# Kernel tuning notes

Hardware: AMD Instinct MI355X
Metric: run time of the kernel (lower is better)

The kernel has to match this reference:

```python
import jax, jax.numpy as jnp
import numpy as np

N = 100000   # nodes
E = 1600000  # edges
IN, H, C = 128, 128, 64
LN_EPS = 1e-5


def _xavier(key, fan_in, fan_out):
    lim = jnp.sqrt(6.0 / (fan_in + fan_out)).astype(jnp.float32)
    return jax.random.uniform(key, (fan_in, fan_out), jnp.float32, -lim, lim)


def setup_inputs() -> dict:
    key = jax.random.key(0)
    ks = jax.random.split(key, 6)
    feats = jax.random.normal(ks[0], (N, IN), jnp.float32)
    src = jax.random.randint(ks[1], (E,), 0, N, jnp.int32)
    dst = jax.random.randint(ks[2], (E,), 0, N, jnp.int32)
    return {
        "feats": feats, "src": src, "dst": dst,
        "W0": _xavier(ks[3], IN, H), "b0": jnp.zeros((H,), jnp.float32),
        "g0": jnp.ones((H,), jnp.float32), "be0": jnp.zeros((H,), jnp.float32),
        "W1": _xavier(ks[4], H, H), "b1": jnp.zeros((H,), jnp.float32),
        "g1": jnp.ones((H,), jnp.float32), "be1": jnp.zeros((H,), jnp.float32),
        "W2": _xavier(ks[5], H, C), "b2": jnp.zeros((C,), jnp.float32),
    }


def _gcn_agg(h, src, dst):
    # symmetric GCN normalization: out[v] = sum_{(u,v) in E} h[u] / sqrt(deg_out(u) * deg_in(v))
    ones = jnp.ones(src.shape, jnp.float32)
    deg_out = jax.ops.segment_sum(ones, src, num_segments=N)
    deg_in = jax.ops.segment_sum(ones, dst, num_segments=N)
    norm_o = jax.lax.rsqrt(jnp.maximum(deg_out, 1.0))
    norm_i = jax.lax.rsqrt(jnp.maximum(deg_in, 1.0))
    msg = (h * norm_o[:, None])[src]                       # [E, d] gather
    agg = jax.ops.segment_sum(msg, dst, num_segments=N)    # [N, d] scatter-add
    return agg * norm_i[:, None]


def _layernorm(x, gamma, beta):
    mu = jnp.mean(x, axis=-1, keepdims=True)
    var = jnp.mean(jnp.square(x - mu), axis=-1, keepdims=True)
    return (x - mu) * jax.lax.rsqrt(var + LN_EPS) * gamma + beta


def reference(feats, src, dst, W0, b0, g0, be0, W1, b1, g1, be1, W2, b2):
    # layer 0: agg -> matmul -> bias -> dropout(eval: identity) -> layernorm -> relu
    h = _gcn_agg(feats, src, dst) @ W0 + b0
    h = jax.nn.relu(_layernorm(h, g0, be0))
    # layer 1
    h = _gcn_agg(h, src, dst) @ W1 + b1
    h = jax.nn.relu(_layernorm(h, g1, be1))
    # final layer: agg -> matmul -> bias
    out = _gcn_agg(h, src, dst) @ W2 + b2
    return out
```

## Files before the change

### kernel.cpp

```cpp
#include <hip/hip_runtime.h>
#include <hip/hip_fp16.h>

constexpr float LN_EPS = 1e-5f;

typedef _Float16 f16x8 __attribute__((ext_vector_type(8)));
typedef float f32x4 __attribute__((ext_vector_type(4)));

__device__ __forceinline__ unsigned short f2h(float f) {
  return __half_as_ushort(__float2half_rn(f));
}
__device__ __forceinline__ unsigned int pk2h(float x, float y) {
  return (unsigned int)f2h(x) | ((unsigned int)f2h(y) << 16);
}
__device__ __forceinline__ __half2 u2h2(unsigned int u) {
  return *reinterpret_cast<__half2*>(&u);
}

#define NPB 256
#define CHUNK 4096

__global__ __launch_bounds__(256) void passA_kernel(
    const int* __restrict__ src, const int* __restrict__ dst,
    int* __restrict__ cntD, int* __restrict__ cntS, int NB, int NBLK, int E) {
  extern __shared__ int sh[];
  for (int j = threadIdx.x; j < 2 * NB; j += 256) sh[j] = 0;
  __syncthreads();
  const int blk = blockIdx.x;
  const int base = blk * CHUNK;
  const int end = min(base + CHUNK, E);
  const int cnt = end - base;
  const int nv = cnt >> 2;
  const int4* d4p = reinterpret_cast<const int4*>(dst + base);
  const int4* s4p = reinterpret_cast<const int4*>(src + base);
  for (int q = threadIdx.x; q < nv; q += 256) {
    int4 d4 = d4p[q];
    int4 s4 = s4p[q];
    atomicAdd(&sh[d4.x >> 8], 1); atomicAdd(&sh[d4.y >> 8], 1);
    atomicAdd(&sh[d4.z >> 8], 1); atomicAdd(&sh[d4.w >> 8], 1);
    atomicAdd(&sh[NB + (s4.x >> 8)], 1); atomicAdd(&sh[NB + (s4.y >> 8)], 1);
    atomicAdd(&sh[NB + (s4.z >> 8)], 1); atomicAdd(&sh[NB + (s4.w >> 8)], 1);
  }
  for (int i = (nv << 2) + threadIdx.x; i < cnt; i += 256) {
    atomicAdd(&sh[dst[base + i] >> 8], 1);
    atomicAdd(&sh[NB + (src[base + i] >> 8)], 1);
  }
  __syncthreads();
  for (int j = threadIdx.x; j < NB; j += 256) {
    cntD[j * NBLK + blk] = sh[j];
    cntS[j * NBLK + blk] = sh[NB + j];
  }
}

__global__ __launch_bounds__(512) void scan1_kernel(
    const int* __restrict__ cntD, const int* __restrict__ cntS,
    int* __restrict__ offLD, int* __restrict__ offLS,
    int* __restrict__ totD, int* __restrict__ totS, int NB, int NBLK) {
  __shared__ int p[512];
  const int t = threadIdx.x;
  const bool isS = blockIdx.x >= NB;
  const int b = isS ? blockIdx.x - NB : blockIdx.x;
  const int* cnt = isS ? cntS : cntD;
  int* offL = isS ? offLS : offLD;
  int own = (t < NBLK) ? cnt[b * NBLK + t] : 0;
  p[t] = own;
  __syncthreads();
  for (int off = 1; off < 512; off <<= 1) {
    int x = (t >= off) ? p[t - off] : 0;
    __syncthreads();
    p[t] += x;
    __syncthreads();
  }
  if (t < NBLK) offL[b * NBLK + t] = p[t] - own;
  if (t == 511) (isS ? totS : totD)[b] = p[511];
}

__global__ __launch_bounds__(512) void scan2_kernel(
    const int* __restrict__ totD, const int* __restrict__ totS,
    int* __restrict__ bktD, int* __restrict__ bktS,
    int* __restrict__ row_st, int NB, int N, int E) {
  __shared__ int p[512];
  const int t = threadIdx.x;
  int own = (t < NB) ? totD[t] : 0;
  p[t] = own;
  __syncthreads();
  for (int off = 1; off < 512; off <<= 1) {
    int x = (t >= off) ? p[t - off] : 0;
    __syncthreads();
    p[t] += x;
    __syncthreads();
  }
  if (t < NB) bktD[t] = p[t] - own;
  __syncthreads();
  int own2 = (t < NB) ? totS[t] : 0;
  p[t] = own2;
  __syncthreads();
  for (int off = 1; off < 512; off <<= 1) {
    int x = (t >= off) ? p[t - off] : 0;
    __syncthreads();
    p[t] += x;
    __syncthreads();
  }
  if (t < NB) bktS[t] = p[t] - own2;
  if (t == 0) {
    bktD[NB] = E;
    bktS[NB] = E;
    row_st[N] = E;
  }
}

__global__ __launch_bounds__(256) void passB_kernel(
    const int* __restrict__ src, const int* __restrict__ dst,
    const int* __restrict__ cntD, const int* __restrict__ cntS,
    const int* __restrict__ offLD, const int* __restrict__ offLS,
    const int* __restrict__ bkt_stD, const int* __restrict__ bkt_stS,
    unsigned int* __restrict__ packedD, unsigned char* __restrict__ srcS,
    int NB, int NBLK, int E) {
  __shared__ unsigned int sD[CHUNK];
  __shared__ unsigned short bD_[CHUNK];
  __shared__ unsigned char sS_[CHUNK];
  __shared__ unsigned short bS_[CHUNK];
  __shared__ int hD[512], lD[512], hS[512], lS[512];
  const int t = threadIdx.x;
  const int blk = blockIdx.x;
  const int base = blk * CHUNK;
  const int end = min(base + CHUNK, E);
  const int cnt = end - base;
  hD[t] = (t < NB) ? cntD[t * NBLK + blk] : 0;
  hD[t + 256] = (t + 256 < NB) ? cntD[(t + 256) * NBLK + blk] : 0;
  hS[t] = (t < NB) ? cntS[t * NBLK + blk] : 0;
  hS[t + 256] = (t + 256 < NB) ? cntS[(t + 256) * NBLK + blk] : 0;
  __syncthreads();
  int oD0 = hD[t], oD1 = hD[t + 256], oS0 = hS[t], oS1 = hS[t + 256];
  for (int off = 1; off < 512; off <<= 1) {
    int xd0 = (t >= off) ? hD[t - off] : 0;
    int xd1 = (t + 256 >= off) ? hD[t + 256 - off] : 0;
    int xs0 = (t >= off) ? hS[t - off] : 0;
    int xs1 = (t + 256 >= off) ? hS[t + 256 - off] : 0;
    __syncthreads();
    hD[t] += xd0; hD[t + 256] += xd1;
    hS[t] += xs0; hS[t + 256] += xs1;
    __syncthreads();
  }
  lD[t] = hD[t] - oD0; lD[t + 256] = hD[t + 256] - oD1;
  lS[t] = hS[t] - oS0; lS[t + 256] = hS[t + 256] - oS1;
  __syncthreads();
  hD[t] = lD[t]; hD[t + 256] = lD[t + 256];
  hS[t] = lS[t]; hS[t + 256] = lS[t + 256];
  __syncthreads();
  const int nv = cnt >> 2;
  const int4* d4p = reinterpret_cast<const int4*>(dst + base);
  const int4* s4p = reinterpret_cast<const int4*>(src + base);
  for (int q = t; q < nv; q += 256) {
    int4 d4 = d4p[q];
    int4 s4 = s4p[q];
#pragma unroll
    for (int k = 0; k < 4; ++k) {
      const int d = (&d4.x)[k];
      const int s = (&s4.x)[k];
      const int bD = d >> 8;
      const int pD = atomicAdd(&hD[bD], 1);
      sD[pD] = ((unsigned int)(d & 255) << 24) | (unsigned int)s;
      bD_[pD] = (unsigned short)bD;
      const int bS = s >> 8;
      const int pS = atomicAdd(&hS[bS], 1);
      sS_[pS] = (unsigned char)(s & 255);
      bS_[pS] = (unsigned short)bS;
    }
  }
  for (int i = (nv << 2) + t; i < cnt; i += 256) {
    const int d = dst[base + i];
    const int s = src[base + i];
    const int bD = d >> 8;
    const int pD = atomicAdd(&hD[bD], 1);
    sD[pD] = ((unsigned int)(d & 255) << 24) | (unsigned int)s;
    bD_[pD] = (unsigned short)bD;
    const int bS = s >> 8;
    const int pS = atomicAdd(&hS[bS], 1);
    sS_[pS] = (unsigned char)(s & 255);
    bS_[pS] = (unsigned short)bS;
  }
  __syncthreads();
  for (int i = t; i < cnt; i += 256) {
    const int bD = bD_[i];
    packedD[bkt_stD[bD] + offLD[bD * NBLK + blk] + (i - lD[bD])] = sD[i];
    const int bS = bS_[i];
    srcS[bkt_stS[bS] + offLS[bS * NBLK + blk] + (i - lS[bS])] = sS_[i];
  }
}

__global__ __launch_bounds__(256) void passC_kernel(
    const unsigned int* __restrict__ packed, const int* __restrict__ bucket_start,
    int* __restrict__ row_st, float* __restrict__ ni,
    int* __restrict__ edge_src, int N) {
  __shared__ int cnt[NPB];
  __shared__ int cur[NPB];
  __shared__ int tmp[NPB];
  const int b = blockIdx.x;
  const int t = threadIdx.x;
  const int v0 = b * NPB;
  const int bs = bucket_start[b];
  const int be = bucket_start[b + 1];
  cnt[t] = 0;
  __syncthreads();
  const int a0 = bs + ((4 - (bs & 3)) & 3);
  const int a1 = a0 + (((be - a0) >> 2) << 2);
  for (int i = bs + t; i < min(a0, be); i += 256)
    atomicAdd(&cnt[packed[i] >> 24], 1);
  const uint4* p4 = reinterpret_cast<const uint4*>(packed + a0);
  const int nv = (a1 - a0) >> 2;
  for (int q = t; q < nv; q += 256) {
    uint4 p = p4[q];
    atomicAdd(&cnt[p.x >> 24], 1); atomicAdd(&cnt[p.y >> 24], 1);
    atomicAdd(&cnt[p.z >> 24], 1); atomicAdd(&cnt[p.w >> 24], 1);
  }
  for (int i = max(a1, bs) + t; i < be; i += 256)
    atomicAdd(&cnt[packed[i] >> 24], 1);
  __syncthreads();
  int own = cnt[t];
  tmp[t] = own;
  __syncthreads();
  for (int off = 1; off < NPB; off <<= 1) {
    int x = (t >= off) ? tmp[t - off] : 0;
    __syncthreads();
    tmp[t] += x;
    __syncthreads();
  }
  const int pref = tmp[t] - own;
  if (v0 + t < N) {
    row_st[v0 + t] = bs + pref;
    ni[v0 + t] = rsqrtf(fmaxf((float)own, 1.0f));
  }
  cur[t] = bs + pref;
  __syncthreads();
  for (int i = bs + t; i < min(a0, be); i += 256) {
    unsigned int p = packed[i];
    int pos = atomicAdd(&cur[p >> 24], 1);
    edge_src[pos] = (int)(p & 0xFFFFFFu);
  }
  for (int q = t; q < nv; q += 256) {
    uint4 p = p4[q];
#pragma unroll
    for (int k = 0; k < 4; ++k) {
      unsigned int pv = (&p.x)[k];
      int pos = atomicAdd(&cur[pv >> 24], 1);
      edge_src[pos] = (int)(pv & 0xFFFFFFu);
    }
  }
  for (int i = max(a1, bs) + t; i < be; i += 256) {
    unsigned int p = packed[i];
    int pos = atomicAdd(&cur[p >> 24], 1);
    edge_src[pos] = (int)(p & 0xFFFFFFu);
  }
}

__global__ __launch_bounds__(256) void passD_kernel(
    const unsigned char* __restrict__ srcS, const int* __restrict__ bkt_stS,
    float* __restrict__ no, int N) {
  __shared__ int cnt[NPB];
  const int b = blockIdx.x;
  const int t = threadIdx.x;
  cnt[t] = 0;
  __syncthreads();
  const int bs = bkt_stS[b];
  const int be = bkt_stS[b + 1];
  for (int i = bs + t; i < be; i += 256)
    atomicAdd(&cnt[srcS[i]], 1);
  __syncthreads();
  const int v = b * NPB + t;
  if (v < N) no[v] = rsqrtf(fmaxf((float)cnt[t], 1.0f));
}

__global__ void wconv_kernel(const float* __restrict__ W, unsigned short* __restrict__ Wt,
                             int K, int C) {
  int i = blockIdx.x * blockDim.x + threadIdx.x;
  if (i < K * C) {
    int k = i / C, c = i - k * C;
    Wt[c * K + k] = f2h(W[i]);
  }
}

__global__ __launch_bounds__(256) void featconv_kernel(const float* __restrict__ F,
                                                       const float* __restrict__ no,
                                                       unsigned short* __restrict__ out, int N) {
  int row = blockIdx.x * 8 + (threadIdx.x >> 5);
  if (row >= N) return;
  int c = (threadIdx.x & 31) * 4;
  float4 v = *reinterpret_cast<const float4*>(F + (size_t)row * 128 + c);
  float nof = no[row];
  uint2 p = {pk2h(v.x * nof, v.y * nof), pk2h(v.z * nof, v.w * nof)};
  *reinterpret_cast<uint2*>(out + (size_t)row * 128 + c) = p;
}

__global__ __launch_bounds__(256) void gather_agg_h(
    const unsigned short* __restrict__ hH, const int* __restrict__ row_start,
    const int* __restrict__ edge_src, const float* __restrict__ ni,
    unsigned short* __restrict__ aggH, int N) {
  const int v = blockIdx.x * 4 + (threadIdx.x >> 6);
  if (v >= N) return;
  const int l = threadIdx.x & 63;
  const int half = l >> 5;
  const int lane = l & 31;
  const int s = row_start[v];
  const int e = row_start[v + 1];
  const int co = 4 * lane;
  const __half2 z = __float2half2_rn(0.f);
  __half2 A0 = z, A1 = z, B0 = z, B1 = z, C0 = z, C1 = z, D0 = z, D1 = z;
  int j = s;
  for (; j + 8 <= e; j += 8) {
    int u0 = edge_src[j + half];
    int u1 = edge_src[j + 2 + half];
    int u2 = edge_src[j + 4 + half];
    int u3 = edge_src[j + 6 + half];
    uint2 p0 = *reinterpret_cast<const uint2*>(hH + (size_t)u0 * 128 + co);
    uint2 p1 = *reinterpret_cast<const uint2*>(hH + (size_t)u1 * 128 + co);
    uint2 p2 = *reinterpret_cast<const uint2*>(hH + (size_t)u2 * 128 + co);
    uint2 p3 = *reinterpret_cast<const uint2*>(hH + (size_t)u3 * 128 + co);
    A0 = __hadd2(A0, u2h2(p0.x)); A1 = __hadd2(A1, u2h2(p0.y));
    B0 = __hadd2(B0, u2h2(p1.x)); B1 = __hadd2(B1, u2h2(p1.y));
    C0 = __hadd2(C0, u2h2(p2.x)); C1 = __hadd2(C1, u2h2(p2.y));
    D0 = __hadd2(D0, u2h2(p3.x)); D1 = __hadd2(D1, u2h2(p3.y));
  }
  for (; j + 2 <= e; j += 2) {
    int u0 = edge_src[j + half];
    uint2 p0 = *reinterpret_cast<const uint2*>(hH + (size_t)u0 * 128 + co);
    A0 = __hadd2(A0, u2h2(p0.x)); A1 = __hadd2(A1, u2h2(p0.y));
  }
  if (j < e && half == 0) {
    int u0 = edge_src[j];
    uint2 p0 = *reinterpret_cast<const uint2*>(hH + (size_t)u0 * 128 + co);
    A0 = __hadd2(A0, u2h2(p0.x)); A1 = __hadd2(A1, u2h2(p0.y));
  }
  float a0 = (__low2float(A0) + __low2float(B0)) + (__low2float(C0) + __low2float(D0));
  float a1 = (__high2float(A0) + __high2float(B0)) + (__high2float(C0) + __high2float(D0));
  float a2 = (__low2float(A1) + __low2float(B1)) + (__low2float(C1) + __low2float(D1));
  float a3 = (__high2float(A1) + __high2float(B1)) + (__high2float(C1) + __high2float(D1));
  a0 += __shfl_xor(a0, 32);
  a1 += __shfl_xor(a1, 32);
  a2 += __shfl_xor(a2, 32);
  a3 += __shfl_xor(a3, 32);
  if (half == 0) {
    const float niv = ni[v];
    uint2 po = {pk2h(a0 * niv, a1 * niv), pk2h(a2 * niv, a3 * niv)};
    *reinterpret_cast<uint2*>(aggH + (size_t)v * 128 + co) = po;
  }
}

__global__ __launch_bounds__(256) void gather_out(
    const unsigned short* __restrict__ zH, const int* __restrict__ row_start,
    const int* __restrict__ edge_src, const float* __restrict__ ni,
    const float* __restrict__ bias, float* __restrict__ out, int N) {
  const int v = blockIdx.x * 4 + (threadIdx.x >> 6);
  if (v >= N) return;
  const int l = threadIdx.x & 63;
  const int half = l >> 5;
  const int lane = l & 31;
  const int s = row_start[v];
  const int e = row_start[v + 1];
  const int co = 2 * lane;
  const __half2 z = __float2half2_rn(0.f);
  __half2 A = z, B = z, C = z, D = z;
  int j = s;
  for (; j + 8 <= e; j += 8) {
    int u0 = edge_src[j + half];
    int u1 = edge_src[j + 2 + half];
    int u2 = edge_src[j + 4 + half];
    int u3 = edge_src[j + 6 + half];
    A = __hadd2(A, u2h2(*reinterpret_cast<const unsigned int*>(zH + (size_t)u0 * 64 + co)));
    B = __hadd2(B, u2h2(*reinterpret_cast<const unsigned int*>(zH + (size_t)u1 * 64 + co)));
    C = __hadd2(C, u2h2(*reinterpret_cast<const unsigned int*>(zH + (size_t)u2 * 64 + co)));
    D = __hadd2(D, u2h2(*reinterpret_cast<const unsigned int*>(zH + (size_t)u3 * 64 + co)));
  }
  for (; j + 2 <= e; j += 2) {
    int u0 = edge_src[j + half];
    A = __hadd2(A, u2h2(*reinterpret_cast<const unsigned int*>(zH + (size_t)u0 * 64 + co)));
  }
  if (j < e && half == 0) {
    int u0 = edge_src[j];
    A = __hadd2(A, u2h2(*reinterpret_cast<const unsigned int*>(zH + (size_t)u0 * 64 + co)));
  }
  float a0 = (__low2float(A) + __low2float(B)) + (__low2float(C) + __low2float(D));
  float a1 = (__high2float(A) + __high2float(B)) + (__high2float(C) + __high2float(D));
  a0 += __shfl_xor(a0, 32);
  a1 += __shfl_xor(a1, 32);
  if (half == 0) {
    const float niv = ni[v];
    float2 bb = *reinterpret_cast<const float2*>(bias + co);
    float2 w = {a0 * niv + bb.x, a1 * niv + bb.y};
    *reinterpret_cast<float2*>(out + (size_t)v * 64 + co) = w;
  }
}

__global__ __launch_bounds__(256) void mm_mfma_ln(
    const unsigned short* __restrict__ A, const unsigned short* __restrict__ Wt,
    const float* __restrict__ b, const float* __restrict__ g,
    const float* __restrict__ be, const float* __restrict__ no,
    unsigned short* __restrict__ out, int N) {
  __shared__ float sS[2][2][16];
  __shared__ float sQ[2][2][16];
  __shared__ float sNo[32];
  const int rbase = blockIdx.x * 32;
  const int w = threadIdx.x >> 6;
  const int l = threadIdx.x & 63;
  const int rt = w & 1, ch = w >> 1;
  if (threadIdx.x < 32) sNo[threadIdx.x] = no[min(rbase + (int)threadIdx.x, N - 1)];
  const int arow = min(rbase + rt * 16 + (l & 15), N - 1);
  const int kof = (l >> 4) * 8;

  f16x8 af[4];
  const unsigned short* ap = A + (size_t)arow * 128 + kof;
#pragma unroll
  for (int kk = 0; kk < 4; ++kk)
    af[kk] = *reinterpret_cast<const f16x8*>(ap + kk * 32);

  f32x4 acc[4] = {};
#pragma unroll
  for (int ct = 0; ct < 4; ++ct) {
    const int ccol = ch * 64 + ct * 16 + (l & 15);
    const unsigned short* bp = Wt + (size_t)ccol * 128 + kof;
#pragma unroll
    for (int kk = 0; kk < 4; ++kk) {
      f16x8 bfr = *reinterpret_cast<const f16x8*>(bp + kk * 32);
      acc[ct] = __builtin_amdgcn_mfma_f32_16x16x32_f16(af[kk], bfr, acc[ct], 0, 0, 0);
    }
  }

  float s[4] = {0.f, 0.f, 0.f, 0.f}, q[4] = {0.f, 0.f, 0.f, 0.f};
#pragma unroll
  for (int ct = 0; ct < 4; ++ct) {
    const float bc = b[ch * 64 + ct * 16 + (l & 15)];
#pragma unroll
    for (int j = 0; j < 4; ++j) {
      float v = acc[ct][j] + bc;
      acc[ct][j] = v;
      s[j] += v;
      q[j] += v * v;
    }
  }
#pragma unroll
  for (int j = 0; j < 4; ++j) {
#pragma unroll
    for (int off = 1; off < 16; off <<= 1) {
      s[j] += __shfl_xor(s[j], off);
      q[j] += __shfl_xor(q[j], off);
    }
  }
  const int grp = l >> 4;
  if ((l & 15) == 0) {
#pragma unroll
    for (int j = 0; j < 4; ++j) {
      sS[rt][ch][grp * 4 + j] = s[j];
      sQ[rt][ch][grp * 4 + j] = q[j];
    }
  }
  __syncthreads();

#pragma unroll
  for (int j = 0; j < 4; ++j) {
    const int r = grp * 4 + j;
    const int row = rbase + rt * 16 + r;
    float S = sS[rt][0][r] + sS[rt][1][r];
    float Q = sQ[rt][0][r] + sQ[rt][1][r];
    float mu = S * (1.f / 128.f);
    float rstd = rsqrtf(fmaxf(Q * (1.f / 128.f) - mu * mu, 0.f) + LN_EPS);
    float nof = sNo[rt * 16 + r];
    if (row < N) {
#pragma unroll
      for (int ct = 0; ct < 4; ++ct) {
        const int ccol = ch * 64 + ct * 16 + (l & 15);
        float y = (acc[ct][j] - mu) * rstd * g[ccol] + be[ccol];
        y = fmaxf(y, 0.f) * nof;
        out[(size_t)row * 128 + ccol] = f2h(y);
      }
    }
  }
}

__global__ __launch_bounds__(256) void mm_z_mfma(
    const unsigned short* __restrict__ A, const unsigned short* __restrict__ Wt,
    unsigned short* __restrict__ zH, int N) {
  const int rbase = blockIdx.x * 32;
  const int w = threadIdx.x >> 6;
  const int l = threadIdx.x & 63;
  const int rt = w & 1, ch = w >> 1;
  const int arow = min(rbase + rt * 16 + (l & 15), N - 1);
  const int kof = (l >> 4) * 8;

  f16x8 af[4];
  const unsigned short* ap = A + (size_t)arow * 128 + kof;
#pragma unroll
  for (int kk = 0; kk < 4; ++kk)
    af[kk] = *reinterpret_cast<const f16x8*>(ap + kk * 32);

  f32x4 acc[2] = {};
#pragma unroll
  for (int ct = 0; ct < 2; ++ct) {
    const int ccol = ch * 32 + ct * 16 + (l & 15);
    const unsigned short* bp = Wt + (size_t)ccol * 128 + kof;
#pragma unroll
    for (int kk = 0; kk < 4; ++kk) {
      f16x8 bfr = *reinterpret_cast<const f16x8*>(bp + kk * 32);
      acc[ct] = __builtin_amdgcn_mfma_f32_16x16x32_f16(af[kk], bfr, acc[ct], 0, 0, 0);
    }
  }
  const int grp = l >> 4;
#pragma unroll
  for (int ct = 0; ct < 2; ++ct) {
    const int ccol = ch * 32 + ct * 16 + (l & 15);
#pragma unroll
    for (int j = 0; j < 4; ++j) {
      const int row = rbase + rt * 16 + grp * 4 + j;
      if (row < N) zH[(size_t)row * 64 + ccol] = f2h(acc[ct][j]);
    }
  }
}

extern "C" void kernel_launch(void* const* d_in, const int* in_sizes, int n_in,
                              void* d_out, int out_size, void* d_ws, size_t ws_size,
                              hipStream_t stream) {
  const float* feats = (const float*)d_in[0];
  const int*   src   = (const int*)d_in[1];
  const int*   dst   = (const int*)d_in[2];
  const float* W0    = (const float*)d_in[3];
  const float* b0    = (const float*)d_in[4];
  const float* g0    = (const float*)d_in[5];
  const float* be0   = (const float*)d_in[6];
  const float* W1    = (const float*)d_in[7];
  const float* b1    = (const float*)d_in[8];
  const float* g1    = (const float*)d_in[9];
  const float* be1   = (const float*)d_in[10];
  const float* W2    = (const float*)d_in[11];
  const float* b2    = (const float*)d_in[12];
  float* out = (float*)d_out;

  const int n = in_sizes[0] / 128;
  const int e = in_sizes[1];
  const int NB = (n + NPB - 1) / NPB;
  const int NBLK = (e + CHUNK - 1) / CHUNK;

  float* ws = (float*)d_ws;
  auto pad4 = [](size_t x) { return (x + 3) & ~(size_t)3; };
  size_t o = 0;
  float* norm_o  = ws + o; o = pad4(o + n);
  float* norm_i  = ws + o; o = pad4(o + n);
  int*   cntD    = (int*)(ws + o); o = pad4(o + (size_t)NB * NBLK);
  int*   cntS    = (int*)(ws + o); o = pad4(o + (size_t)NB * NBLK);
  int*   offLD   = (int*)(ws + o); o = pad4(o + (size_t)NB * NBLK);
  int*   offLS   = (int*)(ws + o); o = pad4(o + (size_t)NB * NBLK);
  int*   totD    = (int*)(ws + o); o = pad4(o + NB);
  int*   totS    = (int*)(ws + o); o = pad4(o + NB);
  int*   bkt_stD = (int*)(ws + o); o = pad4(o + NB + 1);
  int*   bkt_stS = (int*)(ws + o); o = pad4(o + NB + 1);
  int*   row_st  = (int*)(ws + o); o = pad4(o + n + 1);
  unsigned int*  packedD = (unsigned int*)(ws + o);  o = pad4(o + (size_t)e);
  unsigned char* srcS    = (unsigned char*)(ws + o); o = pad4(o + (size_t)(e + 3) / 4);
  int*   edg_src = (int*)(ws + o); o = pad4(o + (size_t)e);
  unsigned short* featH = (unsigned short*)(ws + o); o = pad4(o + (size_t)n * 64);
  unsigned short* aggH  = (unsigned short*)(ws + o); o = pad4(o + (size_t)n * 64);
  unsigned short* Wt0   = (unsigned short*)(ws + o); o = pad4(o + 128 * 128 / 2);
  unsigned short* Wt1   = (unsigned short*)(ws + o); o = pad4(o + 128 * 128 / 2);
  unsigned short* Wt2   = (unsigned short*)(ws + o); o = pad4(o + 128 * 64 / 2);
  unsigned short* hH = featH;
  unsigned short* zH = aggH;

  passA_kernel<<<NBLK, 256, 2 * NB * sizeof(int), stream>>>(src, dst, cntD, cntS, NB, NBLK, e);
  scan1_kernel<<<2 * NB, 512, 0, stream>>>(cntD, cntS, offLD, offLS, totD, totS, NB, NBLK);
  scan2_kernel<<<1, 512, 0, stream>>>(totD, totS, bkt_stD, bkt_stS, row_st, NB, n, e);
  passB_kernel<<<NBLK, 256, 0, stream>>>(src, dst, cntD, cntS, offLD, offLS, bkt_stD, bkt_stS,
                                         packedD, srcS, NB, NBLK, e);
  passC_kernel<<<NB, 256, 0, stream>>>(packedD, bkt_stD, row_st, norm_i, edg_src, n);
  passD_kernel<<<NB, 256, 0, stream>>>(srcS, bkt_stS, norm_o, n);

  wconv_kernel<<<(128 * 128 + 255) / 256, 256, 0, stream>>>(W0, Wt0, 128, 128);
  wconv_kernel<<<(128 * 128 + 255) / 256, 256, 0, stream>>>(W1, Wt1, 128, 128);
  wconv_kernel<<<(128 * 64 + 255) / 256, 256, 0, stream>>>(W2, Wt2, 128, 64);
  featconv_kernel<<<(n + 7) / 8, 256, 0, stream>>>(feats, norm_o, featH, n);

  const int gblocks = (n + 3) / 4;
  const int mblocks = (n + 31) / 32;

  gather_agg_h<<<gblocks, 256, 0, stream>>>(featH, row_st, edg_src, norm_i, aggH, n);
  mm_mfma_ln<<<mblocks, 256, 0, stream>>>(aggH, Wt0, b0, g0, be0, norm_o, hH, n);
  gather_agg_h<<<gblocks, 256, 0, stream>>>(hH, row_st, edg_src, norm_i, aggH, n);
  mm_mfma_ln<<<mblocks, 256, 0, stream>>>(aggH, Wt1, b1, g1, be1, norm_o, hH, n);
  mm_z_mfma<<<mblocks, 256, 0, stream>>>(hH, Wt2, zH, n);
  gather_out<<<gblocks, 256, 0, stream>>>(zH, row_st, edg_src, norm_i, b2, out, n);
}
```

Measured before the change: 388.9 us.

## Slice gathers by feature columns and fuse layer-1 LN with final matmul

Gather kernels now split the feature dimension into 16-column slices, with grid blocks ordered slice-major. Each wave walks 8 nodes with 8 edge groups per node, so concurrently running blocks touch only a narrow slice of the source feature table, which is meant to improve L2 hit rate on random gathers. The layer-1 matmul+LayerNorm is fused with the W2 projection through a shared-memory tile, removing one kernel and a round trip of the hidden activations. In exchange, each edge index is read once per slice and each gather load is only 4 bytes, and the per-node loop is serial with more shuffle reductions.

```diff
diff --git a/kernel.cpp b/kernel.cpp
--- a/kernel.cpp
+++ b/kernel.cpp
@@ -291,102 +291,74 @@
   *reinterpret_cast<uint2*>(out + (size_t)row * 128 + c) = p;
 }
 
-__global__ __launch_bounds__(256) void gather_agg_h(
+__global__ __launch_bounds__(256) void gather_slice(
     const unsigned short* __restrict__ hH, const int* __restrict__ row_start,
     const int* __restrict__ edge_src, const float* __restrict__ ni,
-    unsigned short* __restrict__ aggH, int N) {
-  const int v = blockIdx.x * 4 + (threadIdx.x >> 6);
-  if (v >= N) return;
+    unsigned short* __restrict__ aggH, int N, int gblocks) {
+  const int slice = blockIdx.x / gblocks;
+  const int nb = blockIdx.x - slice * gblocks;
+  const int w = threadIdx.x >> 6;
   const int l = threadIdx.x & 63;
-  const int half = l >> 5;
-  const int lane = l & 31;
-  const int s = row_start[v];
-  const int e = row_start[v + 1];
-  const int co = 4 * lane;
-  const __half2 z = __float2half2_rn(0.f);
-  __half2 A0 = z, A1 = z, B0 = z, B1 = z, C0 = z, C1 = z, D0 = z, D1 = z;
-  int j = s;
-  for (; j + 8 <= e; j += 8) {
-    int u0 = edge_src[j + half];
-    int u1 = edge_src[j + 2 + half];
-    int u2 = edge_src[j + 4 + half];
-    int u3 = edge_src[j + 6 + half];
-    uint2 p0 = *reinterpret_cast<const uint2*>(hH + (size_t)u0 * 128 + co);
-    uint2 p1 = *reinterpret_cast<const uint2*>(hH + (size_t)u1 * 128 + co);
-    uint2 p2 = *reinterpret_cast<const uint2*>(hH + (size_t)u2 * 128 + co);
-    uint2 p3 = *reinterpret_cast<const uint2*>(hH + (size_t)u3 * 128 + co);
-    A0 = __hadd2(A0, u2h2(p0.x)); A1 = __hadd2(A1, u2h2(p0.y));
-    B0 = __hadd2(B0, u2h2(p1.x)); B1 = __hadd2(B1, u2h2(p1.y));
-    C0 = __hadd2(C0, u2h2(p2.x)); C1 = __hadd2(C1, u2h2(p2.y));
-    D0 = __hadd2(D0, u2h2(p3.x)); D1 = __hadd2(D1, u2h2(p3.y));
-  }
-  for (; j + 2 <= e; j += 2) {
-    int u0 = edge_src[j + half];
-    uint2 p0 = *reinterpret_cast<const uint2*>(hH + (size_t)u0 * 128 + co);
-    A0 = __hadd2(A0, u2h2(p0.x)); A1 = __hadd2(A1, u2h2(p0.y));
-  }
-  if (j < e && half == 0) {
-    int u0 = edge_src[j];
-    uint2 p0 = *reinterpret_cast<const uint2*>(hH + (size_t)u0 * 128 + co);
-    A0 = __hadd2(A0, u2h2(p0.x)); A1 = __hadd2(A1, u2h2(p0.y));
-  }
-  float a0 = (__low2float(A0) + __low2float(B0)) + (__low2float(C0) + __low2float(D0));
-  float a1 = (__high2float(A0) + __high2float(B0)) + (__high2float(C0) + __high2float(D0));
-  float a2 = (__low2float(A1) + __low2float(B1)) + (__low2float(C1) + __low2float(D1));
-  float a3 = (__high2float(A1) + __high2float(B1)) + (__high2float(C1) + __high2float(D1));
-  a0 += __shfl_xor(a0, 32);
-  a1 += __shfl_xor(a1, 32);
-  a2 += __shfl_xor(a2, 32);
-  a3 += __shfl_xor(a3, 32);
-  if (half == 0) {
-    const float niv = ni[v];
-    uint2 po = {pk2h(a0 * niv, a1 * niv), pk2h(a2 * niv, a3 * niv)};
-    *reinterpret_cast<uint2*>(aggH + (size_t)v * 128 + co) = po;
-  }
-}
-
-__global__ __launch_bounds__(256) void gather_out(
+  const int grp = l >> 3;
+  const int lane = l & 7;
+  const int co = slice * 16 + lane * 2;
+  const int vbase = nb * 32 + w * 8;
+  const __half2 zz = __float2half2_rn(0.f);
+#pragma unroll 1
+  for (int k = 0; k < 8; ++k) {
+    const int v = vbase + k;
+    if (v >= N) break;
+    const int s = row_start[v];
+    const int e = row_start[v + 1];
+    __half2 acc = zz;
+    for (int j = s + grp; j < e; j += 8)
+      acc = __hadd2(acc, u2h2(*reinterpret_cast<const unsigned int*>(
+                        hH + (size_t)edge_src[j] * 128 + co)));
+    float a0 = __low2float(acc), a1 = __high2float(acc);
+    a0 += __shfl_xor(a0, 8);  a1 += __shfl_xor(a1, 8);
+    a0 += __shfl_xor(a0, 16); a1 += __shfl_xor(a1, 16);
+    a0 += __shfl_xor(a0, 32); a1 += __shfl_xor(a1, 32);
+    if (grp == 0) {
+      const float niv = ni[v];
+      *reinterpret_cast<unsigned int*>(aggH + (size_t)v * 128 + co) =
+          pk2h(a0 * niv, a1 * niv);
+    }
+  }
+}
+
+__global__ __launch_bounds__(256) void gather_out_slice(
     const unsigned short* __restrict__ zH, const int* __restrict__ row_start,
     const int* __restrict__ edge_src, const float* __restrict__ ni,
-    const float* __restrict__ bias, float* __restrict__ out, int N) {
-  const int v = blockIdx.x * 4 + (threadIdx.x >> 6);
-  if (v >= N) return;
+    const float* __restrict__ bias, float* __restrict__ out, int N, int gblocks) {
+  const int slice = blockIdx.x / gblocks;
+  const int nb = blockIdx.x - slice * gblocks;
+  const int w = threadIdx.x >> 6;
   const int l = threadIdx.x & 63;
-  const int half = l >> 5;
-  const int lane = l & 31;
-  const int s = row_start[v];
-  const int e = row_start[v + 1];
-  const int co = 2 * lane;
-  const __half2 z = __float2half2_rn(0.f);
-  __half2 A = z, B = z, C = z, D = z;
-  int j = s;
-  for (; j + 8 <= e; j += 8) {
-    int u0 = edge_src[j + half];
-    int u1 = edge_src[j + 2 + half];
-    int u2 = edge_src[j + 4 + half];
-    int u3 = edge_src[j + 6 + half];
-    A = __hadd2(A, u2h2(*reinterpret_cast<const unsigned int*>(zH + (size_t)u0 * 64 + co)));
-    B = __hadd2(B, u2h2(*reinterpret_cast<const unsigned int*>(zH + (size_t)u1 * 64 + co)));
-    C = __hadd2(C, u2h2(*reinterpret_cast<const unsigned int*>(zH + (size_t)u2 * 64 + co)));
-    D = __hadd2(D, u2h2(*reinterpret_cast<const unsigned int*>(zH + (size_t)u3 * 64 + co)));
-  }
-  for (; j + 2 <= e; j += 2) {
-    int u0 = edge_src[j + half];
-    A = __hadd2(A, u2h2(*reinterpret_cast<const unsigned int*>(zH + (size_t)u0 * 64 + co)));
-  }
-  if (j < e && half == 0) {
-    int u0 = edge_src[j];
-    A = __hadd2(A, u2h2(*reinterpret_cast<const unsigned int*>(zH + (size_t)u0 * 64 + co)));
-  }
-  float a0 = (__low2float(A) + __low2float(B)) + (__low2float(C) + __low2float(D));
-  float a1 = (__high2float(A) + __high2float(B)) + (__high2float(C) + __high2float(D));
-  a0 += __shfl_xor(a0, 32);
-  a1 += __shfl_xor(a1, 32);
-  if (half == 0) {
-    const float niv = ni[v];
-    float2 bb = *reinterpret_cast<const float2*>(bias + co);
-    float2 w = {a0 * niv + bb.x, a1 * niv + bb.y};
-    *reinterpret_cast<float2*>(out + (size_t)v * 64 + co) = w;
+  const int grp = l >> 3;
+  const int lane = l & 7;
+  const int co = slice * 16 + lane * 2;
+  const int vbase = nb * 32 + w * 8;
+  const __half2 zz = __float2half2_rn(0.f);
+#pragma unroll 1
+  for (int k = 0; k < 8; ++k) {
+    const int v = vbase + k;
+    if (v >= N) break;
+    const int s = row_start[v];
+    const int e = row_start[v + 1];
+    __half2 acc = zz;
+    for (int j = s + grp; j < e; j += 8)
+      acc = __hadd2(acc, u2h2(*reinterpret_cast<const unsigned int*>(
+                        zH + (size_t)edge_src[j] * 64 + co)));
+    float a0 = __low2float(acc), a1 = __high2float(acc);
+    a0 += __shfl_xor(a0, 8);  a1 += __shfl_xor(a1, 8);
+    a0 += __shfl_xor(a0, 16); a1 += __shfl_xor(a1, 16);
+    a0 += __shfl_xor(a0, 32); a1 += __shfl_xor(a1, 32);
+    if (grp == 0) {
+      const float niv = ni[v];
+      float2 bb = *reinterpret_cast<const float2*>(bias + co);
+      float2 o = {a0 * niv + bb.x, a1 * niv + bb.y};
+      *reinterpret_cast<float2*>(out + (size_t)v * 64 + co) = o;
+    }
   }
 }
 
@@ -475,13 +447,20 @@
   }
 }
 
-__global__ __launch_bounds__(256) void mm_z_mfma(
+__global__ __launch_bounds__(256) void mm_ln_z(
     const unsigned short* __restrict__ A, const unsigned short* __restrict__ Wt,
-    unsigned short* __restrict__ zH, int N) {
+    const float* __restrict__ b, const float* __restrict__ g,
+    const float* __restrict__ be, const float* __restrict__ no,
+    const unsigned short* __restrict__ Wt2, unsigned short* __restrict__ zH, int N) {
+  __shared__ float sS[2][2][16];
+  __shared__ float sQ[2][2][16];
+  __shared__ float sNo[32];
+  __shared__ unsigned short ht[32][136];
   const int rbase = blockIdx.x * 32;
   const int w = threadIdx.x >> 6;
   const int l = threadIdx.x & 63;
   const int rt = w & 1, ch = w >> 1;
+  if (threadIdx.x < 32) sNo[threadIdx.x] = no[min(rbase + (int)threadIdx.x, N - 1)];
   const int arow = min(rbase + rt * 16 + (l & 15), N - 1);
   const int kof = (l >> 4) * 8;
 
@@ -491,10 +470,10 @@
   for (int kk = 0; kk < 4; ++kk)
     af[kk] = *reinterpret_cast<const f16x8*>(ap + kk * 32);
 
-  f32x4 acc[2] = {};
-#pragma unroll
-  for (int ct = 0; ct < 2; ++ct) {
-    const int ccol = ch * 32 + ct * 16 + (l & 15);
+  f32x4 acc[4] = {};
+#pragma unroll
+  for (int ct = 0; ct < 4; ++ct) {
+    const int ccol = ch * 64 + ct * 16 + (l & 15);
     const unsigned short* bp = Wt + (size_t)ccol * 128 + kof;
 #pragma unroll
     for (int kk = 0; kk < 4; ++kk) {
@@ -502,14 +481,78 @@
       acc[ct] = __builtin_amdgcn_mfma_f32_16x16x32_f16(af[kk], bfr, acc[ct], 0, 0, 0);
     }
   }
+
+  float s[4] = {0.f, 0.f, 0.f, 0.f}, q[4] = {0.f, 0.f, 0.f, 0.f};
+#pragma unroll
+  for (int ct = 0; ct < 4; ++ct) {
+    const float bc = b[ch * 64 + ct * 16 + (l & 15)];
+#pragma unroll
+    for (int j = 0; j < 4; ++j) {
+      float v = acc[ct][j] + bc;
+      acc[ct][j] = v;
+      s[j] += v;
+      q[j] += v * v;
+    }
+  }
+#pragma unroll
+  for (int j = 0; j < 4; ++j) {
+#pragma unroll
+    for (int off = 1; off < 16; off <<= 1) {
+      s[j] += __shfl_xor(s[j], off);
+      q[j] += __shfl_xor(q[j], off);
+    }
+  }
   const int grp = l >> 4;
+  if ((l & 15) == 0) {
+#pragma unroll
+    for (int j = 0; j < 4; ++j) {
+      sS[rt][ch][grp * 4 + j] = s[j];
+      sQ[rt][ch][grp * 4 + j] = q[j];
+    }
+  }
+  __syncthreads();
+
+#pragma unroll
+  for (int j = 0; j < 4; ++j) {
+    const int r = grp * 4 + j;
+    float S = sS[rt][0][r] + sS[rt][1][r];
+    float Q = sQ[rt][0][r] + sQ[rt][1][r];
+    float mu = S * (1.f / 128.f);
+    float rstd = rsqrtf(fmaxf(Q * (1.f / 128.f) - mu * mu, 0.f) + LN_EPS);
+    float nof = sNo[rt * 16 + r];
+#pragma unroll
+    for (int ct = 0; ct < 4; ++ct) {
+      const int ccol = ch * 64 + ct * 16 + (l & 15);
+      float y = (acc[ct][j] - mu) * rstd * g[ccol] + be[ccol];
+      y = fmaxf(y, 0.f) * nof;
+      ht[rt * 16 + r][ccol] = f2h(y);
+    }
+  }
+  __syncthreads();
+
+  f16x8 af2[4];
+#pragma unroll
+  for (int kk = 0; kk < 4; ++kk)
+    af2[kk] = *reinterpret_cast<const f16x8*>(&ht[rt * 16 + (l & 15)][kof + kk * 32]);
+
+  f32x4 acc2[2] = {};
 #pragma unroll
   for (int ct = 0; ct < 2; ++ct) {
     const int ccol = ch * 32 + ct * 16 + (l & 15);
+    const unsigned short* bp = Wt2 + (size_t)ccol * 128 + kof;
+#pragma unroll
+    for (int kk = 0; kk < 4; ++kk) {
+      f16x8 bfr = *reinterpret_cast<const f16x8*>(bp + kk * 32);
+      acc2[ct] = __builtin_amdgcn_mfma_f32_16x16x32_f16(af2[kk], bfr, acc2[ct], 0, 0, 0);
+    }
+  }
+#pragma unroll
+  for (int ct = 0; ct < 2; ++ct) {
+    const int ccol = ch * 32 + ct * 16 + (l & 15);
 #pragma unroll
     for (int j = 0; j < 4; ++j) {
       const int row = rbase + rt * 16 + grp * 4 + j;
-      if (row < N) zH[(size_t)row * 64 + ccol] = f2h(acc[ct][j]);
+      if (row < N) zH[(size_t)row * 64 + ccol] = f2h(acc2[ct][j]);
     }
   }
 }
@@ -556,11 +599,11 @@
   int*   edg_src = (int*)(ws + o); o = pad4(o + (size_t)e);
   unsigned short* featH = (unsigned short*)(ws + o); o = pad4(o + (size_t)n * 64);
   unsigned short* aggH  = (unsigned short*)(ws + o); o = pad4(o + (size_t)n * 64);
+  unsigned short* zH    = (unsigned short*)(ws + o); o = pad4(o + (size_t)n * 32);
   unsigned short* Wt0   = (unsigned short*)(ws + o); o = pad4(o + 128 * 128 / 2);
   unsigned short* Wt1   = (unsigned short*)(ws + o); o = pad4(o + 128 * 128 / 2);
   unsigned short* Wt2   = (unsigned short*)(ws + o); o = pad4(o + 128 * 64 / 2);
   unsigned short* hH = featH;
-  unsigned short* zH = aggH;
 
   passA_kernel<<<NBLK, 256, 2 * NB * sizeof(int), stream>>>(src, dst, cntD, cntS, NB, NBLK, e);
   scan1_kernel<<<2 * NB, 512, 0, stream>>>(cntD, cntS, offLD, offLS, totD, totS, NB, NBLK);
@@ -575,13 +618,12 @@
   wconv_kernel<<<(128 * 64 + 255) / 256, 256, 0, stream>>>(W2, Wt2, 128, 64);
   featconv_kernel<<<(n + 7) / 8, 256, 0, stream>>>(feats, norm_o, featH, n);
 
-  const int gblocks = (n + 3) / 4;
+  const int g32 = (n + 31) / 32;
   const int mblocks = (n + 31) / 32;
 
-  gather_agg_h<<<gblocks, 256, 0, stream>>>(featH, row_st, edg_src, norm_i, aggH, n);
+  gather_slice<<<g32 * 8, 256, 0, stream>>>(featH, row_st, edg_src, norm_i, aggH, n, g32);
   mm_mfma_ln<<<mblocks, 256, 0, stream>>>(aggH, Wt0, b0, g0, be0, norm_o, hH, n);
-  gather_agg_h<<<gblocks, 256, 0, stream>>>(hH, row_st, edg_src, norm_i, aggH, n);
-  mm_mfma_ln<<<mblocks, 256, 0, stream>>>(aggH, Wt1, b1, g1, be1, norm_o, hH, n);
-  mm_z_mfma<<<mblocks, 256, 0, stream>>>(hH, Wt2, zH, n);
-  gather_out<<<gblocks, 256, 0, stream>>>(zH, row_st, edg_src, norm_i, b2, out, n);
-}
+  gather_slice<<<g32 * 8, 256, 0, stream>>>(hH, row_st, edg_src, norm_i, aggH, n, g32);
+  mm_ln_z<<<mblocks, 256, 0, stream>>>(aggH, Wt1, b1, g1, be1, norm_o, Wt2, zH, n);
+  gather_out_slice<<<g32 * 4, 256, 0, stream>>>(zH, row_st, edg_src, norm_i, b2, out, n, g32);
+}
```

New measurement: 883.4 us. 2.27x slower.
